# Kernel optimization log

Measured on AMD Instinct MI355X. Metric: run time of the kernel, lower is better.

The kernel has to match this reference:

```python
import jax, jax.numpy as jnp
import numpy as np

B, S, H = 32, 1024, 768          # batch, seq_len, bert hidden
E, W, P = 128, 8, 512            # entities/sample, span width, rel pairs/sample
NT, NR = 5, 9                    # entity types, relation types
D1, HEADS1, D2, RD = 128, 2, 64, 32
REL_IN = 2 * D2 + RD + H         # 928


def _layernorm(x, g, b):
    m = x.mean(-1, keepdims=True)
    v = x.var(-1, keepdims=True)
    return (x - m) * jax.lax.rsqrt(v + 1e-5) * g + b


def _gat_dense(x, Wm, a_src, a_dst, bias, concat):
    # Fully-connected entity graph (incl. self-loops, PyG GATConv default).
    Bn, En, _ = x.shape
    Hh, D = a_src.shape
    h = (x @ Wm).reshape(Bn, En, Hh, D)                      # [B,E,h,D]
    s = jnp.einsum('behd,hd->beh', h, a_src)                 # source score
    d = jnp.einsum('behd,hd->beh', h, a_dst)                 # target score
    # edge j->i : e_ij = leaky_relu(s_j + d_i)
    e = jax.nn.leaky_relu(d[:, :, None, :] + s[:, None, :, :], 0.2)  # [B,i,j,h]
    alpha = jax.nn.softmax(e, axis=2)
    o = jnp.einsum('bijh,bjhd->bihd', alpha, h)
    o = o.reshape(Bn, En, Hh * D) if concat else o.mean(axis=2)
    return o + bias


def setup_inputs() -> dict:
    key = jax.random.key(0)
    ks = jax.random.split(key, 20)
    f = lambda k, shape: jax.random.normal(k, shape, jnp.float32) * 0.02
    return dict(
        sequence_output=jax.random.normal(ks[0], (B, S, H), jnp.float32),
        entity_starts=jax.random.randint(ks[1], (B, E), 0, S - W),
        entity_type_ids=jax.random.randint(ks[2], (B, E), 0, NT),
        pair_idx=jax.random.randint(ks[3], (B, P, 2), 0, E),
        rel_type_ids=jax.random.randint(ks[4], (B, P), 0, NR),
        entity_type_emb=f(ks[5], (NT, H)),
        rel_type_emb=f(ks[6], (NR, RD)),
        W1=f(ks[7], (H, HEADS1 * D1)), a_src1=f(ks[8], (HEADS1, D1)),
        a_dst1=f(ks[9], (HEADS1, D1)), b1=jnp.zeros((HEADS1 * D1,), jnp.float32),
        ln1_g=jnp.ones((HEADS1 * D1,), jnp.float32), ln1_b=jnp.zeros((HEADS1 * D1,), jnp.float32),
        W2=f(ks[10], (HEADS1 * D1, D2)), a_src2=f(ks[11], (1, D2)),
        a_dst2=f(ks[12], (1, D2)), b2=jnp.zeros((D2,), jnp.float32),
        ln2_g=jnp.ones((D2,), jnp.float32), ln2_b=jnp.zeros((D2,), jnp.float32),
        Wr1=f(ks[13], (REL_IN, 256)), br1=jnp.zeros((256,), jnp.float32),
        Wr2=f(ks[14], (256, 1)), br2=jnp.zeros((1,), jnp.float32),
    )


def reference(sequence_output, entity_starts, entity_type_ids, pair_idx, rel_type_ids,
              entity_type_emb, rel_type_emb,
              W1, a_src1, a_dst1, b1, ln1_g, ln1_b,
              W2, a_src2, a_dst2, b2, ln2_g, ln2_b,
              Wr1, br1, Wr2, br2):
    bidx = jnp.arange(B)[:, None]
    # --- per-entity attention pooling over span tokens ---
    tok_idx = entity_starts[:, :, None] + jnp.arange(W)            # [B,E,W]
    toks = sequence_output[jnp.arange(B)[:, None, None], tok_idx]  # [B,E,W,H]
    mean = toks.mean(axis=2)                                       # [B,E,H]
    attn = jax.nn.softmax(jnp.einsum('bewh,beh->bew', toks, mean), axis=-1)
    pooled = jnp.einsum('bew,bewh->beh', attn, toks)
    x = pooled + entity_type_emb[entity_type_ids]                  # [B,E,H]
    # --- 2-layer GAT over fully-connected entity graph ---
    x = jax.nn.elu(_layernorm(_gat_dense(x, W1, a_src1, a_dst1, b1, True), ln1_g, ln1_b))
    x = jax.nn.elu(_layernorm(_gat_dense(x, W2, a_src2, a_dst2, b2, False), ln2_g, ln2_b))
    # --- gather-concat relation MLP scoring ---
    cls = sequence_output[:, 0, :]                                 # [B,H]
    x1 = x[bidx, pair_idx[:, :, 0]]                                # [B,P,64]
    x2 = x[bidx, pair_idx[:, :, 1]]
    rel = rel_type_emb[rel_type_ids]                               # [B,P,32]
    pv = jnp.concatenate([x1, x2, rel, jnp.broadcast_to(cls[:, None, :], (B, P, H))], axis=-1)
    scores = (jax.nn.relu(pv @ Wr1 + br1) @ Wr2 + br2)[..., 0]     # [B,P]
    return scores
```

## Files before the change

kernel.cpp:

```cpp
#include <hip/hip_runtime.h>
#include <hip/hip_bf16.h>

#define BB 32
#define SS 1024
#define HHH 768
#define EE 128
#define WW 8
#define PP 512
#define ND1 128
#define NH1 2
#define ND2 64
#define RDD 32

typedef __attribute__((ext_vector_type(8))) short bf16x8;
typedef __attribute__((ext_vector_type(8))) unsigned short us8;
typedef __attribute__((ext_vector_type(4))) float f32x4;

__device__ __forceinline__ unsigned short f2bf(float v) {
    __hip_bfloat16 h = __float2bfloat16(v);
    return *(unsigned short*)&h;
}
__device__ __forceinline__ float bf2f(unsigned short u) {
    unsigned int x = ((unsigned int)u) << 16;
    float f; __builtin_memcpy(&f, &x, 4);
    return f;
}

__global__ __launch_bounds__(256) void pool_kernel(
    const float* __restrict__ seq, const int* __restrict__ starts,
    const int* __restrict__ types, const float* __restrict__ temb,
    const float* __restrict__ br1, float* __restrict__ baseo,
    unsigned short* __restrict__ xout) {
    int be = blockIdx.x;
    int b = be >> 7;
    int tid = threadIdx.x;
    __shared__ float toks[WW][HHH];
    __shared__ float scred[WW];
    __shared__ float attn_s[WW];

    if (be < BB) baseo[(size_t)be * 256 + tid] = br1[tid];

    int start = starts[be];
    const float4* bp4 = (const float4*)(seq + ((size_t)b * SS + start) * HHH);
    for (int idx = tid; idx < WW * (HHH / 4); idx += 256) {
        int w = idx / (HHH / 4), h4 = idx % (HHH / 4);
        float4 v = bp4[(size_t)w * (HHH / 4) + h4];
        toks[w][h4 * 4 + 0] = v.x; toks[w][h4 * 4 + 1] = v.y;
        toks[w][h4 * 4 + 2] = v.z; toks[w][h4 * 4 + 3] = v.w;
    }
    __syncthreads();

    float sc[WW];
#pragma unroll
    for (int w = 0; w < WW; w++) sc[w] = 0.f;
#pragma unroll
    for (int c = 0; c < 3; c++) {
        int h = tid + 256 * c;
        float s = 0.f;
#pragma unroll
        for (int w = 0; w < WW; w++) s += toks[w][h];
        float m = s * (1.0f / WW);
#pragma unroll
        for (int w = 0; w < WW; w++) sc[w] += toks[w][h] * m;
    }
    if (tid < WW) scred[tid] = 0.f;
    __syncthreads();
    int lane = tid & 63;
#pragma unroll
    for (int w = 0; w < WW; w++) {
        float v = sc[w];
        for (int o = 32; o > 0; o >>= 1) v += __shfl_down(v, o, 64);
        if (lane == 0) atomicAdd(&scred[w], v);
    }
    __syncthreads();
    if (tid == 0) {
        float mx = scred[0];
        for (int w = 1; w < WW; w++) mx = fmaxf(mx, scred[w]);
        float ssum = 0.f;
        float a[WW];
        for (int w = 0; w < WW; w++) { a[w] = __expf(scred[w] - mx); ssum += a[w]; }
        float inv = 1.f / ssum;
        for (int w = 0; w < WW; w++) attn_s[w] = a[w] * inv;
    }
    __syncthreads();

    int t = types[be];
    const float* emb = temb + (size_t)t * HHH;
#pragma unroll
    for (int c = 0; c < 3; c++) {
        int h = tid + 256 * c;
        float p = 0.f;
#pragma unroll
        for (int w = 0; w < WW; w++) p += attn_s[w] * toks[w][h];
        xout[(size_t)be * HHH + h] = f2bf(p + emb[h]);
    }
}

__global__ __launch_bounds__(256) void prep_kernel(
    const float* __restrict__ W1, unsigned short* __restrict__ Wt,
    const float* __restrict__ Wr1, unsigned short* __restrict__ Wtr,
    const float* __restrict__ W2, unsigned short* __restrict__ W2t,
    const float* __restrict__ seq, float* __restrict__ baseo) {
    int blk = blockIdx.x;
    int tid = threadIdx.x;
    __shared__ float wbuf[16][256];
    if (blk < 48) {
        int k0 = blk * 16;
        for (int i = tid; i < 16 * 256; i += 256)
            wbuf[i >> 8][i & 255] = W1[(size_t)(k0 + (i >> 8)) * 256 + (i & 255)];
        __syncthreads();
        int n = tid;
        us8 v0, v1;
#pragma unroll
        for (int kk = 0; kk < 8; kk++) v0[kk] = f2bf(wbuf[kk][n]);
#pragma unroll
        for (int kk = 0; kk < 8; kk++) v1[kk] = f2bf(wbuf[8 + kk][n]);
        *(us8*)(Wt + (size_t)n * HHH + k0) = v0;
        *(us8*)(Wt + (size_t)n * HHH + k0 + 8) = v1;
    } else if (blk < 58) {
        int k0 = (blk - 48) * 16;
        for (int i = tid; i < 16 * 256; i += 256)
            wbuf[i >> 8][i & 255] = Wr1[(size_t)(k0 + (i >> 8)) * 256 + (i & 255)];
        __syncthreads();
        int n = tid;
        us8 v0, v1;
#pragma unroll
        for (int kk = 0; kk < 8; kk++) v0[kk] = f2bf(wbuf[kk][n]);
#pragma unroll
        for (int kk = 0; kk < 8; kk++) v1[kk] = f2bf(wbuf[8 + kk][n]);
        *(us8*)(Wtr + (size_t)n * 160 + k0) = v0;
        *(us8*)(Wtr + (size_t)n * 160 + k0 + 8) = v1;
    } else if (blk < 74) {
        int k0 = (blk - 58) * 16;
        for (int i = tid; i < 16 * 64; i += 256)
            wbuf[i >> 6][i & 63] = W2[(size_t)(k0 + (i >> 6)) * 64 + (i & 63)];
        __syncthreads();
        if (tid < 64) {
            int n = tid;
            us8 v0, v1;
#pragma unroll
            for (int kk = 0; kk < 8; kk++) v0[kk] = f2bf(wbuf[kk][n]);
#pragma unroll
            for (int kk = 0; kk < 8; kk++) v1[kk] = f2bf(wbuf[8 + kk][n]);
            *(us8*)(W2t + (size_t)n * 256 + k0) = v0;
            *(us8*)(W2t + (size_t)n * 256 + k0 + 8) = v1;
        }
    } else {
        int pc = blk - 74;
        int kc = pc % 12;
        int b = pc / 12;
        int n = tid;
        __shared__ float cls[64];
        if (n < 64) cls[n] = seq[(size_t)b * SS * HHH + kc * 64 + n];
        __syncthreads();
        float acc = 0.f;
        const float* w = Wr1 + (size_t)(160 + kc * 64) * 256 + n;
#pragma unroll 16
        for (int k = 0; k < 64; k++) acc += cls[k] * w[(size_t)k * 256];
        atomicAdd(&baseo[(size_t)b * 256 + n], acc);
    }
}

__global__ __launch_bounds__(256) void gemm1_mfma_kernel(
    const unsigned short* __restrict__ Xb, const unsigned short* __restrict__ Wt,
    float* __restrict__ C) {
    const int K = HHH;
    int n0 = blockIdx.x * 64;
    int m0 = blockIdx.y * 64;
    int tid = threadIdx.x;
    int wave = tid >> 6, lane = tid & 63;
    int wm = (wave >> 1) * 32, wn = (wave & 1) * 32;

    __shared__ __align__(16) unsigned short As[64][40];
    __shared__ __align__(16) unsigned short Bs[64][40];

    f32x4 acc[2][2] = {};
    int ar = tid >> 2;
    int ac = (tid & 3) * 8;
    int fr = lane & 15;
    int fk = (lane >> 4) * 8;

    for (int k0 = 0; k0 < K; k0 += 32) {
        us8 av = *(const us8*)(Xb + (size_t)(m0 + ar) * K + k0 + ac);
        us8 bv = *(const us8*)(Wt + (size_t)(n0 + ar) * K + k0 + ac);
        *(us8*)(&As[ar][ac]) = av;
        *(us8*)(&Bs[ar][ac]) = bv;
        __syncthreads();

        bf16x8 a0 = *(const bf16x8*)(&As[wm + fr][fk]);
        bf16x8 a1 = *(const bf16x8*)(&As[wm + 16 + fr][fk]);
        bf16x8 b0 = *(const bf16x8*)(&Bs[wn + fr][fk]);
        bf16x8 b1 = *(const bf16x8*)(&Bs[wn + 16 + fr][fk]);

        acc[0][0] = __builtin_amdgcn_mfma_f32_16x16x32_bf16(a0, b0, acc[0][0], 0, 0, 0);
        acc[0][1] = __builtin_amdgcn_mfma_f32_16x16x32_bf16(a0, b1, acc[0][1], 0, 0, 0);
        acc[1][0] = __builtin_amdgcn_mfma_f32_16x16x32_bf16(a1, b0, acc[1][0], 0, 0, 0);
        acc[1][1] = __builtin_amdgcn_mfma_f32_16x16x32_bf16(a1, b1, acc[1][1], 0, 0, 0);
        __syncthreads();
    }

    int crow = (lane >> 4) * 4;
    int ccol = lane & 15;
#pragma unroll
    for (int mi = 0; mi < 2; mi++)
#pragma unroll
        for (int ni = 0; ni < 2; ni++)
#pragma unroll
            for (int r = 0; r < 4; r++)
                C[(size_t)(m0 + wm + mi * 16 + crow + r) * 256 +
                  n0 + wn + ni * 16 + ccol] = acc[mi][ni][r];
}

__global__ void sd1_kernel(const float* __restrict__ h1, const float* __restrict__ asrc,
                           const float* __restrict__ adst, float* __restrict__ s1,
                           float* __restrict__ d1) {
    int beh = blockIdx.x;
    int h = beh & 1;
    int be = beh >> 1;
    int lane = threadIdx.x;
    const float* row = h1 + (size_t)be * 256 + h * 128;
    float v0 = row[lane], v1 = row[lane + 64];
    float ss = v0 * asrc[h * 128 + lane] + v1 * asrc[h * 128 + lane + 64];
    float dd = v0 * adst[h * 128 + lane] + v1 * adst[h * 128 + lane + 64];
    for (int o = 32; o > 0; o >>= 1) {
        ss += __shfl_down(ss, o, 64);
        dd += __shfl_down(dd, o, 64);
    }
    if (lane == 0) { s1[beh] = ss; d1[beh] = dd; }
}

__global__ __launch_bounds__(256) void gat1_ln_kernel(
    const float* __restrict__ h1, const float* __restrict__ s1,
    const float* __restrict__ d1, const float* __restrict__ b1,
    const float* __restrict__ gamma, const float* __restrict__ beta,
    unsigned short* __restrict__ g1b) {
    int bi = blockIdx.x;
    int b = bi >> 7;
    int tid = threadIdx.x;
    int h = tid >> 7;
    int jj = tid & 127;
    int lane = tid & 63, wid = tid >> 6;
    __shared__ float alpha[2][128];
    __shared__ float red[4];

    float di = d1[bi * 2 + h];
    float sj = s1[((size_t)b * 128 + jj) * 2 + h];
    float ev = di + sj;
    ev = ev >= 0.f ? ev : 0.2f * ev;

    float mx = ev;
    for (int o = 32; o > 0; o >>= 1) mx = fmaxf(mx, __shfl_down(mx, o, 64));
    if (lane == 0) red[wid] = mx;
    __syncthreads();
    mx = fmaxf(red[h * 2], red[h * 2 + 1]);
    __syncthreads();
    float ex = __expf(ev - mx);
    float sm = ex;
    for (int o = 32; o > 0; o >>= 1) sm += __shfl_down(sm, o, 64);
    if (lane == 0) red[wid] = sm;
    __syncthreads();
    sm = red[h * 2] + red[h * 2 + 1];
    alpha[h][jj] = ex / sm;
    __syncthreads();

    const float* hb = h1 + (size_t)b * 128 * 256 + tid;
    float o = 0.f;
#pragma unroll 8
    for (int j = 0; j < 128; j++) o += alpha[h][j] * hb[(size_t)j * 256];
    o += b1[tid];

    float s = o;
    for (int off = 32; off > 0; off >>= 1) s += __shfl_down(s, off, 64);
    if (lane == 0) red[wid] = s;
    __syncthreads();
    float mean = (red[0] + red[1] + red[2] + red[3]) * (1.f / 256.f);
    __syncthreads();
    float dv = o - mean;
    float sq = dv * dv;
    for (int off = 32; off > 0; off >>= 1) sq += __shfl_down(sq, off, 64);
    if (lane == 0) red[wid] = sq;
    __syncthreads();
    float var = (red[0] + red[1] + red[2] + red[3]) * (1.f / 256.f);
    float y = dv * rsqrtf(var + 1e-5f) * gamma[tid] + beta[tid];
    y = y > 0.f ? y : (__expf(y) - 1.f);
    g1b[(size_t)bi * 256 + tid] = f2bf(y);
}

__global__ __launch_bounds__(256) void gemm2_mfma_kernel(
    const unsigned short* __restrict__ g1b, const unsigned short* __restrict__ W2t,
    const float* __restrict__ asrc, const float* __restrict__ adst,
    float* __restrict__ h2, float* __restrict__ s2, float* __restrict__ d2) {
    int m0 = blockIdx.x * 64;
    int tid = threadIdx.x;
    int wave = tid >> 6, lane = tid & 63;
    int wm = (wave >> 1) * 32, wn = (wave & 1) * 32;

    __shared__ __align__(16) unsigned short As[64][72];
    __shared__ __align__(16) unsigned short Bs[64][72];
    __shared__ float sdred[64][2][2];

    f32x4 acc[2][2] = {};
    int fr = lane & 15;
    int fk = (lane >> 4) * 8;

    for (int kc = 0; kc < 4; kc++) {
        for (int it = 0; it < 2; it++) {
            int i = tid + it * 256;
            int row = i >> 3, c = i & 7;
            *(us8*)(&As[row][c * 8]) =
                *(const us8*)(g1b + (size_t)(m0 + row) * 256 + kc * 64 + c * 8);
            *(us8*)(&Bs[row][c * 8]) =
                *(const us8*)(W2t + (size_t)row * 256 + kc * 64 + c * 8);
        }
        __syncthreads();
#pragma unroll
        for (int ks = 0; ks < 2; ks++) {
            int kb = ks * 32 + fk;
            bf16x8 a0 = *(const bf16x8*)(&As[wm + fr][kb]);
            bf16x8 a1 = *(const bf16x8*)(&As[wm + 16 + fr][kb]);
            bf16x8 b0 = *(const bf16x8*)(&Bs[wn + fr][kb]);
            bf16x8 b1 = *(const bf16x8*)(&Bs[wn + 16 + fr][kb]);
            acc[0][0] = __builtin_amdgcn_mfma_f32_16x16x32_bf16(a0, b0, acc[0][0], 0, 0, 0);
            acc[0][1] = __builtin_amdgcn_mfma_f32_16x16x32_bf16(a0, b1, acc[0][1], 0, 0, 0);
            acc[1][0] = __builtin_amdgcn_mfma_f32_16x16x32_bf16(a1, b0, acc[1][0], 0, 0, 0);
            acc[1][1] = __builtin_amdgcn_mfma_f32_16x16x32_bf16(a1, b1, acc[1][1], 0, 0, 0);
        }
        __syncthreads();
    }

    int crow = (lane >> 4) * 4;
    int ccol = lane & 15;
    float asv[2], adv[2];
#pragma unroll
    for (int ni = 0; ni < 2; ni++) {
        int n = wn + ni * 16 + ccol;
        asv[ni] = asrc[n];
        adv[ni] = adst[n];
    }
#pragma unroll
    for (int mi = 0; mi < 2; mi++) {
#pragma unroll
        for (int r = 0; r < 4; r++) {
            float sp = 0.f, dp = 0.f;
#pragma unroll
            for (int ni = 0; ni < 2; ni++) {
                float v = acc[mi][ni][r];
                h2[(size_t)(m0 + wm + mi * 16 + crow + r) * 64 +
                   wn + ni * 16 + ccol] = v;
                sp += v * asv[ni];
                dp += v * adv[ni];
            }
            for (int msk = 1; msk < 16; msk <<= 1) {
                sp += __shfl_xor(sp, msk, 64);
                dp += __shfl_xor(dp, msk, 64);
            }
            if ((lane & 15) == 0) {
                int row = wm + mi * 16 + crow + r;
                sdred[row][wn >> 5][0] = sp;
                sdred[row][wn >> 5][1] = dp;
            }
        }
    }
    __syncthreads();
    if (tid < 64 && wave == 0) {
        s2[m0 + tid] = sdred[tid][0][0] + sdred[tid][1][0];
        d2[m0 + tid] = sdred[tid][0][1] + sdred[tid][1][1];
    }
}

__global__ __launch_bounds__(128) void gat2_kernel(
    const float* __restrict__ h2, const float* __restrict__ s2,
    const float* __restrict__ d2, const float* __restrict__ b2v,
    const float* __restrict__ gamma, const float* __restrict__ beta,
    float* __restrict__ x2) {
    int bi = blockIdx.x;
    int b = bi >> 7;
    int tid = threadIdx.x;
    __shared__ float alpha[128];
    __shared__ float red[2];

    float ev = d2[bi] + s2[(size_t)b * 128 + tid];
    ev = ev >= 0.f ? ev : 0.2f * ev;
    float mx = ev;
    for (int o = 32; o > 0; o >>= 1) mx = fmaxf(mx, __shfl_down(mx, o, 64));
    int lane = tid & 63, wid = tid >> 6;
    if (lane == 0) red[wid] = mx;
    __syncthreads();
    mx = fmaxf(red[0], red[1]);
    __syncthreads();
    float ex = __expf(ev - mx);
    float sm = ex;
    for (int o = 32; o > 0; o >>= 1) sm += __shfl_down(sm, o, 64);
    if (lane == 0) red[wid] = sm;
    __syncthreads();
    sm = red[0] + red[1];
    alpha[tid] = ex / sm;
    __syncthreads();

    if (tid < 64) {
        const float* hb = h2 + (size_t)b * 128 * 64 + tid;
        float o = 0.f;
#pragma unroll 8
        for (int j = 0; j < 128; j++) o += alpha[j] * hb[(size_t)j * 64];
        o += b2v[tid];
        float s = o;
        for (int off = 32; off > 0; off >>= 1) s += __shfl_down(s, off, 64);
        s = __shfl(s, 0, 64);
        float mean = s * (1.f / 64.f);
        float dv = o - mean;
        float sq = dv * dv;
        for (int off = 32; off > 0; off >>= 1) sq += __shfl_down(sq, off, 64);
        sq = __shfl(sq, 0, 64);
        float var = sq * (1.f / 64.f);
        float y = dv * rsqrtf(var + 1e-5f) * gamma[tid] + beta[tid];
        y = y > 0.f ? y : (__expf(y) - 1.f);
        x2[(size_t)bi * 64 + tid] = y;
    }
}

__global__ __launch_bounds__(256) void score_mfma_kernel(
    const float* __restrict__ x2, const float* __restrict__ baseo,
    const int* __restrict__ pair_idx, const int* __restrict__ rel_ids,
    const float* __restrict__ rel_emb, const unsigned short* __restrict__ Wtr,
    const float* __restrict__ Wr2, const float* __restrict__ br2,
    float* __restrict__ out) {
    int blk = blockIdx.x;
    int b = blk >> 3;
    int p0 = (blk & 7) * 64;
    int tid = threadIdx.x;
    int wave = tid >> 6, lane = tid & 63;
    int wn = wave * 64;

    __shared__ __align__(16) unsigned short As[64][168];
    __shared__ __align__(16) unsigned short Bs[256][40];
    __shared__ float sred[64][4];
    __shared__ int prs[64][3];

    if (tid < 64) {
        int p = p0 + tid;
        prs[tid][0] = pair_idx[((size_t)b * PP + p) * 2 + 0];
        prs[tid][1] = pair_idx[((size_t)b * PP + p) * 2 + 1];
        prs[tid][2] = rel_ids[(size_t)b * PP + p];
    }
    __syncthreads();
    for (int it = 0; it < 40; it++) {
        int i = tid + it * 256;
        int m = i / 160, k = i % 160;
        float v;
        if (k < 64) v = x2[((size_t)b * EE + prs[m][0]) * 64 + k];
        else if (k < 128) v = x2[((size_t)b * EE + prs[m][1]) * 64 + (k - 64)];
        else v = rel_emb[prs[m][2] * RDD + (k - 128)];
        As[m][k] = f2bf(v);
    }

    f32x4 acc[4][4] = {};
    int fr = lane & 15;
    int fk = (lane >> 4) * 8;

    for (int kc = 0; kc < 5; kc++) {
        for (int it = 0; it < 4; it++) {
            int i = tid + it * 256;
            int n = i >> 2, c = i & 3;
            *(us8*)(&Bs[n][c * 8]) =
                *(const us8*)(Wtr + (size_t)n * 160 + kc * 32 + c * 8);
        }
        __syncthreads();
        bf16x8 a[4], bv[4];
#pragma unroll
        for (int mi = 0; mi < 4; mi++)
            a[mi] = *(const bf16x8*)(&As[mi * 16 + fr][kc * 32 + fk]);
#pragma unroll
        for (int ni = 0; ni < 4; ni++)
            bv[ni] = *(const bf16x8*)(&Bs[wn + ni * 16 + fr][fk]);
#pragma unroll
        for (int mi = 0; mi < 4; mi++)
#pragma unroll
            for (int ni = 0; ni < 4; ni++)
                acc[mi][ni] = __builtin_amdgcn_mfma_f32_16x16x32_bf16(
                    a[mi], bv[ni], acc[mi][ni], 0, 0, 0);
        __syncthreads();
    }

    int crow = (lane >> 4) * 4;
    int ccol = lane & 15;
    float basev[4], w2v[4];
#pragma unroll
    for (int ni = 0; ni < 4; ni++) {
        int n = wn + ni * 16 + ccol;
        basev[ni] = baseo[(size_t)b * 256 + n];
        w2v[ni] = Wr2[n];
    }
#pragma unroll
    for (int mi = 0; mi < 4; mi++) {
#pragma unroll
        for (int r = 0; r < 4; r++) {
            float p = 0.f;
#pragma unroll
            for (int ni = 0; ni < 4; ni++)
                p += fmaxf(acc[mi][ni][r] + basev[ni], 0.f) * w2v[ni];
            for (int msk = 1; msk < 16; msk <<= 1)
                p += __shfl_xor(p, msk, 64);
            if ((lane & 15) == 0)
                sred[mi * 16 + crow + r][wave] = p;
        }
    }
    __syncthreads();
    if (tid < 64) {
        float s = sred[tid][0] + sred[tid][1] + sred[tid][2] + sred[tid][3] + br2[0];
        out[(size_t)b * PP + p0 + tid] = s;
    }
}

extern "C" void kernel_launch(void* const* d_in, const int* in_sizes, int n_in,
                              void* d_out, int out_size, void* d_ws, size_t ws_size,
                              hipStream_t stream) {
    (void)in_sizes; (void)n_in; (void)out_size; (void)ws_size;
    const float* seq      = (const float*)d_in[0];
    const int*   starts   = (const int*)d_in[1];
    const int*   types    = (const int*)d_in[2];
    const int*   pair_idx = (const int*)d_in[3];
    const int*   rel_ids  = (const int*)d_in[4];
    const float* temb     = (const float*)d_in[5];
    const float* remb     = (const float*)d_in[6];
    const float* W1       = (const float*)d_in[7];
    const float* a_src1   = (const float*)d_in[8];
    const float* a_dst1   = (const float*)d_in[9];
    const float* b1       = (const float*)d_in[10];
    const float* ln1_g    = (const float*)d_in[11];
    const float* ln1_b    = (const float*)d_in[12];
    const float* W2       = (const float*)d_in[13];
    const float* a_src2   = (const float*)d_in[14];
    const float* a_dst2   = (const float*)d_in[15];
    const float* b2       = (const float*)d_in[16];
    const float* ln2_g    = (const float*)d_in[17];
    const float* ln2_b    = (const float*)d_in[18];
    const float* Wr1      = (const float*)d_in[19];
    const float* br1      = (const float*)d_in[20];
    const float* Wr2      = (const float*)d_in[21];
    const float* br2      = (const float*)d_in[22];
    float* out = (float*)d_out;

    unsigned short* xb  = (unsigned short*)d_ws;
    unsigned short* Wt  = xb + (size_t)4096 * 768;
    unsigned short* Wtr = Wt + (size_t)256 * 768;
    unsigned short* W2t = Wtr + (size_t)256 * 160;
    unsigned short* g1b = W2t + (size_t)64 * 256;
    float* fbase = (float*)(g1b + (size_t)4096 * 256);
    float* h1   = fbase;
    float* s1   = h1 + (size_t)4096 * 256;
    float* d1   = s1 + 8192;
    float* h2   = d1 + 8192;
    float* s2   = h2 + (size_t)4096 * 64;
    float* d2   = s2 + 4096;
    float* x2   = d2 + 4096;
    float* baseo = x2 + (size_t)4096 * 64;

    pool_kernel<<<BB * EE, 256, 0, stream>>>(seq, starts, types, temb, br1, baseo, xb);
    prep_kernel<<<74 + 12 * 32, 256, 0, stream>>>(W1, Wt, Wr1, Wtr, W2, W2t, seq, baseo);
    gemm1_mfma_kernel<<<dim3(4, 64), 256, 0, stream>>>(xb, Wt, h1);
    sd1_kernel<<<BB * EE * 2, 64, 0, stream>>>(h1, a_src1, a_dst1, s1, d1);
    gat1_ln_kernel<<<BB * EE, 256, 0, stream>>>(h1, s1, d1, b1, ln1_g, ln1_b, g1b);
    gemm2_mfma_kernel<<<64, 256, 0, stream>>>(g1b, W2t, a_src2, a_dst2, h2, s2, d2);
    gat2_kernel<<<BB * EE, 128, 0, stream>>>(h2, s2, d2, b2, ln2_g, ln2_b, x2);
    score_mfma_kernel<<<BB * PP / 64, 256, 0, stream>>>(x2, baseo, pair_idx, rel_ids,
                                                        remb, Wtr, Wr2, br2, out);
}
```

Before: 274.6 us.

## Fuse GAT layer-1 scores and attention aggregation into per-batch-head MFMA kernel

Replaces the separate score kernel and the per-row attention kernel with one kernel per (batch, head). It loads the 128x128 h1 slice into LDS as a bf16 transpose, computes source and destination scores, builds the softmax rows in registers and runs the alpha·h product on MFMA. Before this, each row block re-read the whole batch's h1 from global memory, so h1 was read about 128 times per batch. LayerNorm and ELU move to a separate small kernel that reads an fp32 intermediate. In exchange, the fused kernel launches only 64 blocks, the score dot products use bf16-rounded h1, and there is an extra round trip through global memory for the pre-norm output.

```diff
diff --git a/kernel.cpp b/kernel.cpp
--- a/kernel.cpp
+++ b/kernel.cpp
@@ -211,79 +211,137 @@
                   n0 + wn + ni * 16 + ccol] = acc[mi][ni][r];
 }
 
-__global__ void sd1_kernel(const float* __restrict__ h1, const float* __restrict__ asrc,
-                           const float* __restrict__ adst, float* __restrict__ s1,
-                           float* __restrict__ d1) {
-    int beh = blockIdx.x;
-    int h = beh & 1;
-    int be = beh >> 1;
-    int lane = threadIdx.x;
-    const float* row = h1 + (size_t)be * 256 + h * 128;
-    float v0 = row[lane], v1 = row[lane + 64];
-    float ss = v0 * asrc[h * 128 + lane] + v1 * asrc[h * 128 + lane + 64];
-    float dd = v0 * adst[h * 128 + lane] + v1 * adst[h * 128 + lane + 64];
-    for (int o = 32; o > 0; o >>= 1) {
-        ss += __shfl_down(ss, o, 64);
-        dd += __shfl_down(dd, o, 64);
-    }
-    if (lane == 0) { s1[beh] = ss; d1[beh] = dd; }
-}
-
-__global__ __launch_bounds__(256) void gat1_ln_kernel(
-    const float* __restrict__ h1, const float* __restrict__ s1,
-    const float* __restrict__ d1, const float* __restrict__ b1,
+__global__ __launch_bounds__(256) void gat1_fused_kernel(
+    const float* __restrict__ h1, const float* __restrict__ a_src1,
+    const float* __restrict__ a_dst1, float* __restrict__ g1pre) {
+    int b = blockIdx.x >> 1;
+    int h = blockIdx.x & 1;
+    int tid = threadIdx.x;
+    int wave = tid >> 6, lane = tid & 63;
+    int wm = wave * 32;
+    int fr = lane & 15;
+    int fk = (lane >> 4) * 8;
+
+    __shared__ __align__(16) unsigned short h1T[128][136];
+    __shared__ float s_sh[128];
+    __shared__ float dd_sh[128];
+
+    {
+        int d = tid & 127;
+        int mb = (tid >> 7) * 8;
+        const float* hsrc = h1 + ((size_t)b * 128) * 256 + h * 128 + d;
+#pragma unroll
+        for (int m = 0; m < 8; m++) {
+            int j0 = (mb + m) * 8;
+            us8 pk;
+#pragma unroll
+            for (int jj = 0; jj < 8; jj++)
+                pk[jj] = f2bf(hsrc[(size_t)(j0 + jj) * 256]);
+            *(us8*)(&h1T[d][j0]) = pk;
+        }
+    }
+    __syncthreads();
+
+    {
+        int j = tid & 127;
+        const float* av = (tid < 128) ? (a_src1 + h * 128) : (a_dst1 + h * 128);
+        float accd = 0.f;
+        for (int d2 = 0; d2 < 128; d2++)
+            accd += bf2f(h1T[d2][j]) * av[d2];
+        if (tid < 128) s_sh[j] = accd;
+        else dd_sh[j] = accd;
+    }
+    __syncthreads();
+
+    bf16x8 afrag[2][4];
+#pragma unroll
+    for (int mi = 0; mi < 2; mi++) {
+        int i = wm + mi * 16 + fr;
+        float dd = dd_sh[i];
+        float ev[4][8];
+        float mx = -1e30f;
+#pragma unroll
+        for (int ks = 0; ks < 4; ks++)
+#pragma unroll
+            for (int jj = 0; jj < 8; jj++) {
+                float e = dd + s_sh[ks * 32 + fk + jj];
+                e = e >= 0.f ? e : 0.2f * e;
+                ev[ks][jj] = e;
+                mx = fmaxf(mx, e);
+            }
+        mx = fmaxf(mx, __shfl_xor(mx, 16, 64));
+        mx = fmaxf(mx, __shfl_xor(mx, 32, 64));
+        float sm = 0.f;
+#pragma unroll
+        for (int ks = 0; ks < 4; ks++)
+#pragma unroll
+            for (int jj = 0; jj < 8; jj++) {
+                float e = __expf(ev[ks][jj] - mx);
+                ev[ks][jj] = e;
+                sm += e;
+            }
+        sm += __shfl_xor(sm, 16, 64);
+        sm += __shfl_xor(sm, 32, 64);
+        float inv = 1.f / sm;
+#pragma unroll
+        for (int ks = 0; ks < 4; ks++) {
+            bf16x8 a;
+#pragma unroll
+            for (int jj = 0; jj < 8; jj++)
+                a[jj] = (short)f2bf(ev[ks][jj] * inv);
+            afrag[mi][ks] = a;
+        }
+    }
+
+    f32x4 acc[2][8] = {};
+#pragma unroll
+    for (int ks = 0; ks < 4; ks++) {
+#pragma unroll
+        for (int ni = 0; ni < 8; ni++) {
+            bf16x8 bv = *(const bf16x8*)(&h1T[ni * 16 + fr][ks * 32 + fk]);
+            acc[0][ni] = __builtin_amdgcn_mfma_f32_16x16x32_bf16(
+                afrag[0][ks], bv, acc[0][ni], 0, 0, 0);
+            acc[1][ni] = __builtin_amdgcn_mfma_f32_16x16x32_bf16(
+                afrag[1][ks], bv, acc[1][ni], 0, 0, 0);
+        }
+    }
+
+    int crow = (lane >> 4) * 4;
+    int ccol = lane & 15;
+#pragma unroll
+    for (int mi = 0; mi < 2; mi++)
+#pragma unroll
+        for (int ni = 0; ni < 8; ni++)
+#pragma unroll
+            for (int r = 0; r < 4; r++)
+                g1pre[(size_t)(b * 128 + wm + mi * 16 + crow + r) * 256 +
+                      h * 128 + ni * 16 + ccol] = acc[mi][ni][r];
+}
+
+__global__ __launch_bounds__(256) void ln_elu256b_kernel(
+    const float* __restrict__ g1pre, const float* __restrict__ b1,
     const float* __restrict__ gamma, const float* __restrict__ beta,
     unsigned short* __restrict__ g1b) {
-    int bi = blockIdx.x;
-    int b = bi >> 7;
-    int tid = threadIdx.x;
-    int h = tid >> 7;
-    int jj = tid & 127;
+    int row = blockIdx.x;
+    int tid = threadIdx.x;
+    __shared__ float red[4];
+    float v = g1pre[(size_t)row * 256 + tid] + b1[tid];
+    float s = v;
+    for (int o = 32; o > 0; o >>= 1) s += __shfl_down(s, o, 64);
     int lane = tid & 63, wid = tid >> 6;
-    __shared__ float alpha[2][128];
-    __shared__ float red[4];
-
-    float di = d1[bi * 2 + h];
-    float sj = s1[((size_t)b * 128 + jj) * 2 + h];
-    float ev = di + sj;
-    ev = ev >= 0.f ? ev : 0.2f * ev;
-
-    float mx = ev;
-    for (int o = 32; o > 0; o >>= 1) mx = fmaxf(mx, __shfl_down(mx, o, 64));
-    if (lane == 0) red[wid] = mx;
-    __syncthreads();
-    mx = fmaxf(red[h * 2], red[h * 2 + 1]);
-    __syncthreads();
-    float ex = __expf(ev - mx);
-    float sm = ex;
-    for (int o = 32; o > 0; o >>= 1) sm += __shfl_down(sm, o, 64);
-    if (lane == 0) red[wid] = sm;
-    __syncthreads();
-    sm = red[h * 2] + red[h * 2 + 1];
-    alpha[h][jj] = ex / sm;
-    __syncthreads();
-
-    const float* hb = h1 + (size_t)b * 128 * 256 + tid;
-    float o = 0.f;
-#pragma unroll 8
-    for (int j = 0; j < 128; j++) o += alpha[h][j] * hb[(size_t)j * 256];
-    o += b1[tid];
-
-    float s = o;
-    for (int off = 32; off > 0; off >>= 1) s += __shfl_down(s, off, 64);
     if (lane == 0) red[wid] = s;
     __syncthreads();
     float mean = (red[0] + red[1] + red[2] + red[3]) * (1.f / 256.f);
     __syncthreads();
-    float dv = o - mean;
+    float dv = v - mean;
     float sq = dv * dv;
-    for (int off = 32; off > 0; off >>= 1) sq += __shfl_down(sq, off, 64);
+    for (int o = 32; o > 0; o >>= 1) sq += __shfl_down(sq, o, 64);
     if (lane == 0) red[wid] = sq;
     __syncthreads();
     float var = (red[0] + red[1] + red[2] + red[3]) * (1.f / 256.f);
     float y = dv * rsqrtf(var + 1e-5f) * gamma[tid] + beta[tid];
     y = y > 0.f ? y : (__expf(y) - 1.f);
-    g1b[(size_t)bi * 256 + tid] = f2bf(y);
+    g1b[(size_t)row * 256 + tid] = f2bf(y);
 }
 
 __global__ __launch_bounds__(256) void gemm2_mfma_kernel(
@@ -546,20 +604,19 @@
     unsigned short* W2t = Wtr + (size_t)256 * 160;
     unsigned short* g1b = W2t + (size_t)64 * 256;
     float* fbase = (float*)(g1b + (size_t)4096 * 256);
-    float* h1   = fbase;
-    float* s1   = h1 + (size_t)4096 * 256;
-    float* d1   = s1 + 8192;
-    float* h2   = d1 + 8192;
-    float* s2   = h2 + (size_t)4096 * 64;
-    float* d2   = s2 + 4096;
-    float* x2   = d2 + 4096;
+    float* h1    = fbase;
+    float* g1pre = h1 + (size_t)4096 * 256;
+    float* h2    = g1pre + (size_t)4096 * 256;
+    float* s2    = h2 + (size_t)4096 * 64;
+    float* d2    = s2 + 4096;
+    float* x2    = d2 + 4096;
     float* baseo = x2 + (size_t)4096 * 64;
 
     pool_kernel<<<BB * EE, 256, 0, stream>>>(seq, starts, types, temb, br1, baseo, xb);
     prep_kernel<<<74 + 12 * 32, 256, 0, stream>>>(W1, Wt, Wr1, Wtr, W2, W2t, seq, baseo);
     gemm1_mfma_kernel<<<dim3(4, 64), 256, 0, stream>>>(xb, Wt, h1);
-    sd1_kernel<<<BB * EE * 2, 64, 0, stream>>>(h1, a_src1, a_dst1, s1, d1);
-    gat1_ln_kernel<<<BB * EE, 256, 0, stream>>>(h1, s1, d1, b1, ln1_g, ln1_b, g1b);
+    gat1_fused_kernel<<<BB * 2, 256, 0, stream>>>(h1, a_src1, a_dst1, g1pre);
+    ln_elu256b_kernel<<<BB * EE, 256, 0, stream>>>(g1pre, b1, ln1_g, ln1_b, g1b);
     gemm2_mfma_kernel<<<64, 256, 0, stream>>>(g1b, W2t, a_src2, a_dst2, h2, s2, d2);
     gat2_kernel<<<BB * EE, 128, 0, stream>>>(h2, s2, d2, b2, ln2_g, ln2_b, x2);
     score_mfma_kernel<<<BB * PP / 64, 256, 0, stream>>>(x2, baseo, pair_idx, rel_ids,
```

Result: faster. 260.2 us (-5.2%).
